# Kernel tuning notes

Measured on AMD Instinct MI355X. Metric: run time of the kernel, lower is better.

## Reference

```python
import jax, jax.numpy as jnp
import numpy as np

H = 8
D_MODEL = 512
D_K = D_MODEL // H
NEG = -1e9


def setup_inputs() -> dict:
    key = jax.random.key(0)
    ks = jax.random.split(key, 11)
    B, S = 2, 2048
    scale = 1.0 / np.sqrt(D_MODEL)
    inp = {
        'query': jax.random.normal(ks[0], (B, S, D_MODEL), dtype=jnp.float32),
        'key': jax.random.normal(ks[1], (B, S, D_MODEL), dtype=jnp.float32),
        'value': jax.random.normal(ks[2], (B, S, D_MODEL), dtype=jnp.float32),
        'Wq': jax.random.normal(ks[3], (D_MODEL, D_MODEL), dtype=jnp.float32) * scale,
        'bq': jnp.zeros((D_MODEL,), dtype=jnp.float32),
        'Wk': jax.random.normal(ks[4], (D_MODEL, D_MODEL), dtype=jnp.float32) * scale,
        'bk': jnp.zeros((D_MODEL,), dtype=jnp.float32),
        'Wv': jax.random.normal(ks[5], (D_MODEL, D_MODEL), dtype=jnp.float32) * scale,
        'bv': jnp.zeros((D_MODEL,), dtype=jnp.float32),
        'Wo': jax.random.normal(ks[6], (D_MODEL, D_MODEL), dtype=jnp.float32) * scale,
        'bo': jnp.zeros((D_MODEL,), dtype=jnp.float32),
    }
    return inp


def reference(query, key, value, Wq, bq, Wk, bk, Wv, bv, Wo, bo):
    B, S, _ = query.shape
    # QKV projections (nn.Linear: x @ W.T + b), split into heads -> [B, H, S, D_K]
    def proj(x, W, b):
        return (x @ W.T + b).reshape(B, S, H, D_K).transpose(0, 2, 1, 3)

    q = proj(query, Wq, bq)
    k = proj(key, Wk, bk)
    v = proj(value, Wv, bv)

    scores = jnp.einsum('bhqd,bhkd->bhqk', q, k) / jnp.sqrt(jnp.float32(D_K))
    # diagonal mask (mask=True): token cannot attend to itself
    diag = jnp.eye(S, dtype=bool)
    scores = jnp.where(diag, NEG, scores)

    p_attn = jax.nn.softmax(scores, axis=-1)  # [B, H, S, S]
    x = jnp.einsum('bhqk,bhkd->bhqd', p_attn, v)
    x = x.transpose(0, 2, 1, 3).reshape(B, S, H * D_K)
    return x @ Wo.T + bo
```

## Files before the change

### kernel.cpp

```cpp
#include <hip/hip_runtime.h>
#include <hip/hip_bf16.h>
#include <math.h>

#define NUM_H 8
#define DK    64
#define DM    512
#define SEQ   2048
#define NB    2
#define MROWS (NB*SEQ)

typedef unsigned short u16;
typedef unsigned int   u32;
typedef __attribute__((ext_vector_type(8))) __bf16 bf16x8;
typedef __attribute__((ext_vector_type(4))) float  f32x4;

__device__ __forceinline__ u16 f2bf(float v) {
    union { float f; u32 i; } x; x.f = v;
    u32 r = (x.i + 0x7FFFu + ((x.i >> 16) & 1u)) >> 16;
    return (u16)r;
}
__device__ __forceinline__ u16 f2h(float v) {
    union { _Float16 h; u16 u; } x; x.h = (_Float16)v; return x.u;
}
__device__ __forceinline__ float h2f(u16 u) {
    union { u16 u; _Float16 h; } x; x.u = u; return (float)x.h;
}
__device__ __forceinline__ bf16x8 ld_bf8(const u16* p) {
    union { uint4 u; bf16x8 v; } t;
    t.u = *(const uint4*)p;
    return t.v;
}
__device__ __forceinline__ uint4 pack8bf(const float* f) {
    uint4 o;
    o.x = (u32)f2bf(f[0]) | ((u32)f2bf(f[1]) << 16);
    o.y = (u32)f2bf(f[2]) | ((u32)f2bf(f[3]) << 16);
    o.z = (u32)f2bf(f[4]) | ((u32)f2bf(f[5]) << 16);
    o.w = (u32)f2bf(f[6]) | ((u32)f2bf(f[7]) << 16);
    return o;
}

__global__ __launch_bounds__(256) void convW(
    const float* __restrict__ Wq, const float* __restrict__ Wk,
    const float* __restrict__ Wv, const float* __restrict__ Wo,
    u16* __restrict__ Wscr)
{
    const int z = blockIdx.y;
    const float* src = (z == 0) ? Wq : (z == 1) ? Wk : (z == 2) ? Wv : Wo;
    u16* dst = Wscr + (size_t)z * 262144;
    int i = (blockIdx.x * 256 + threadIdx.x) * 8;
    float4 a = *(const float4*)(src + i);
    float4 b = *(const float4*)(src + i + 4);
    float f[8] = {a.x, a.y, a.z, a.w, b.x, b.y, b.z, b.w};
    *(uint4*)&dst[i] = pack8bf(f);
}

#define MODE_QK 0
#define MODE_VT 1
#define MODE_FIN 2

template<int MODE, bool INBF>
__device__ __forceinline__ void gemm_core(
    const void* __restrict__ Xv, const u16* __restrict__ Wb,
    const float* __restrict__ bias, void* __restrict__ outv,
    u16* As, u16* Bs, int row0, int col0)
{
    const int tid = threadIdx.x;
    const int lane = tid & 63, w = tid >> 6;
    const int ln15 = lane & 15, quad = lane >> 4;
    const int wm = (w >> 1) * 32, wn = (w & 1) * 32;

    f32x4 acc[2][2];
#pragma unroll
    for (int mt = 0; mt < 2; ++mt)
#pragma unroll
        for (int nt = 0; nt < 2; ++nt) acc[mt][nt] = (f32x4){0.f, 0.f, 0.f, 0.f};

    for (int kt = 0; kt < DM; kt += 64) {
        __syncthreads();
#pragma unroll
        for (int g = 0; g < 2; ++g) {
            int idx = g * 2048 + tid * 8;
            int r = idx >> 6, c = idx & 63;
            if (INBF) {
                *(uint4*)&As[r * 72 + c] =
                    *(const uint4*)((const u16*)Xv + (size_t)(row0 + r) * DM + kt + c);
            } else {
                const float* xp = (const float*)Xv + (size_t)(row0 + r) * DM + kt + c;
                float4 a = *(const float4*)xp;
                float4 b2 = *(const float4*)(xp + 4);
                float f[8] = {a.x, a.y, a.z, a.w, b2.x, b2.y, b2.z, b2.w};
                *(uint4*)&As[r * 72 + c] = pack8bf(f);
            }
        }
#pragma unroll
        for (int g = 0; g < 2; ++g) {
            int idx = g * 2048 + tid * 8;
            int r = idx >> 6, c = idx & 63;
            *(uint4*)&Bs[r * 72 + c] =
                *(const uint4*)(Wb + (size_t)(col0 + r) * DM + kt + c);
        }
        __syncthreads();

#pragma unroll
        for (int ks = 0; ks < 2; ++ks) {
            bf16x8 af[2], bfr[2];
#pragma unroll
            for (int mt = 0; mt < 2; ++mt)
                af[mt] = ld_bf8(&As[(wm + mt * 16 + ln15) * 72 + ks * 32 + quad * 8]);
#pragma unroll
            for (int nt = 0; nt < 2; ++nt)
                bfr[nt] = ld_bf8(&Bs[(wn + nt * 16 + ln15) * 72 + ks * 32 + quad * 8]);
#pragma unroll
            for (int mt = 0; mt < 2; ++mt)
#pragma unroll
                for (int nt = 0; nt < 2; ++nt)
                    acc[mt][nt] = __builtin_amdgcn_mfma_f32_16x16x32_bf16(
                        af[mt], bfr[nt], acc[mt][nt], 0, 0, 0);
        }
    }

    float bc[2];
#pragma unroll
    for (int nt = 0; nt < 2; ++nt) bc[nt] = bias[col0 + wn + nt * 16 + ln15];
    const int h = col0 >> 6;

    if (MODE == MODE_FIN) {
        float* outF = (float*)outv;
#pragma unroll
        for (int mt = 0; mt < 2; ++mt)
#pragma unroll
            for (int r = 0; r < 4; ++r) {
                int m = row0 + wm + mt * 16 + quad * 4 + r;
#pragma unroll
                for (int nt = 0; nt < 2; ++nt)
                    outF[(size_t)m * DM + col0 + wn + nt * 16 + ln15] = acc[mt][nt][r] + bc[nt];
            }
    } else if (MODE == MODE_QK) {
        u16* outB = (u16*)outv;
#pragma unroll
        for (int mt = 0; mt < 2; ++mt)
#pragma unroll
            for (int r = 0; r < 4; ++r) {
                int m = row0 + wm + mt * 16 + quad * 4 + r;
                int b = m >> 11, s2 = m & (SEQ - 1);
#pragma unroll
                for (int nt = 0; nt < 2; ++nt) {
                    int dk = wn + nt * 16 + ln15;
                    outB[((size_t)((b * NUM_H + h) * SEQ + s2)) * DK + dk] =
                        f2bf(acc[mt][nt][r] + bc[nt]);
                }
            }
    } else {
        u16* outB = (u16*)outv;
        __syncthreads();
#pragma unroll
        for (int mt = 0; mt < 2; ++mt)
#pragma unroll
            for (int nt = 0; nt < 2; ++nt) {
                int dk = wn + nt * 16 + ln15;
#pragma unroll
                for (int r = 0; r < 4; ++r) {
                    int sl = wm + mt * 16 + quad * 4 + r;
                    As[dk * 72 + sl] = f2bf(acc[mt][nt][r] + bc[nt]);
                }
            }
        __syncthreads();
        int dk = tid >> 2, ch = (tid & 3) * 16;
        int b = row0 >> 11, s0 = row0 & (SEQ - 1);
        size_t base = ((size_t)((b * NUM_H + h) * DK + dk)) * SEQ + s0 + ch;
        *(uint4*)&outB[base]     = *(const uint4*)&As[dk * 72 + ch];
        *(uint4*)&outB[base + 8] = *(const uint4*)&As[dk * 72 + ch + 8];
    }
}

__global__ __launch_bounds__(256) void qkv_mfma(
    const float* __restrict__ xq, const float* __restrict__ xk, const float* __restrict__ xv,
    const u16* __restrict__ Wscr,
    const float* __restrict__ b0, const float* __restrict__ b1, const float* __restrict__ b2,
    u16* __restrict__ oQ, u16* __restrict__ oK, u16* __restrict__ oVt)
{
    __shared__ u16 As[64 * 72];
    __shared__ u16 Bs[64 * 72];
    const int row0 = blockIdx.x * 64, col0 = blockIdx.y * 64;
    const int z = blockIdx.z;
    const u16* W = Wscr + (size_t)z * 262144;
    if (z == 2)
        gemm_core<MODE_VT, false>(xv, W, b2, oVt, As, Bs, row0, col0);
    else if (z == 0)
        gemm_core<MODE_QK, false>(xq, W, b0, oQ, As, Bs, row0, col0);
    else
        gemm_core<MODE_QK, false>(xk, W, b1, oK, As, Bs, row0, col0);
}

__global__ __launch_bounds__(256) void final_mfma(
    const u16* __restrict__ X, const u16* __restrict__ Wbf,
    const float* __restrict__ bias, float* __restrict__ out)
{
    __shared__ u16 As[64 * 72];
    __shared__ u16 Bs[64 * 72];
    gemm_core<MODE_FIN, true>(X, Wbf, bias, out, As, Bs,
                              blockIdx.x * 64, blockIdx.y * 64);
}

#define LSTR 72
__global__ __launch_bounds__(256) void attn_mfma(
    const u16* __restrict__ Qg, const u16* __restrict__ Kg,
    const u16* __restrict__ Vtg, u16* __restrict__ Pd, float* __restrict__ Cl)
{
    __shared__ u16 Klds[64 * LSTR];
    __shared__ u16 Vtlds[64 * LSTR];
    __shared__ u16 Pls[64 * LSTR];

    const int tid = threadIdx.x;
    const int lane = tid & 63;
    const int w = tid >> 6;
    const int ln15 = lane & 15;
    const int quad = lane >> 4;
    const int bh = blockIdx.y;
    const int b = bh >> 3, h = bh & 7;
    const int qb = blockIdx.x * 64;
    const int z = blockIdx.z;
    const int k0 = z * (SEQ / 2), k1 = k0 + SEQ / 2;

    const u16* Qp = Qg + (size_t)bh * SEQ * DK;
    const u16* Kp = Kg + (size_t)bh * SEQ * DK;
    const u16* Vp = Vtg + (size_t)bh * DK * SEQ;

    const int qrowA = qb + w * 16 + ln15;
    const bf16x8 qa0 = ld_bf8(&Qp[(size_t)qrowA * DK + quad * 8]);
    const bf16x8 qa1 = ld_bf8(&Qp[(size_t)qrowA * DK + 32 + quad * 8]);

    f32x4 O[4];
    float l_i[4] = {0.f, 0.f, 0.f, 0.f};
#pragma unroll
    for (int nt = 0; nt < 4; ++nt) O[nt] = (f32x4){0.f, 0.f, 0.f, 0.f};

    const int sr = tid >> 3;
    const int scl = (tid & 7) * 8;

    for (int kt = k0; kt < k1; kt += 64) {
        __syncthreads();
        *(uint4*)&Klds[sr * LSTR + scl]         = *(const uint4*)&Kp[(size_t)(kt + sr) * DK + scl];
        *(uint4*)&Klds[(sr + 32) * LSTR + scl]  = *(const uint4*)&Kp[(size_t)(kt + sr + 32) * DK + scl];
        *(uint4*)&Vtlds[sr * LSTR + scl]        = *(const uint4*)&Vp[(size_t)sr * SEQ + kt + scl];
        *(uint4*)&Vtlds[(sr + 32) * LSTR + scl] = *(const uint4*)&Vp[(size_t)(sr + 32) * SEQ + kt + scl];
        __syncthreads();

        const bool diagt = (kt == qb);
#pragma unroll
        for (int nt2 = 0; nt2 < 4; ++nt2) {
            bf16x8 kb0 = ld_bf8(&Klds[(nt2 * 16 + ln15) * LSTR + quad * 8]);
            bf16x8 kb1 = ld_bf8(&Klds[(nt2 * 16 + ln15) * LSTR + 32 + quad * 8]);
            f32x4 zacc = (f32x4){0.f, 0.f, 0.f, 0.f};
            zacc = __builtin_amdgcn_mfma_f32_16x16x32_bf16(qa0, kb0, zacc, 0, 0, 0);
            zacc = __builtin_amdgcn_mfma_f32_16x16x32_bf16(qa1, kb1, zacc, 0, 0, 0);
#pragma unroll
            for (int r = 0; r < 4; ++r) {
                float e = __expf(fmaf(zacc[r], 0.125f, -4.0f));
                if (diagt && (nt2 * 16 + ln15 == w * 16 + quad * 4 + r)) e = 0.f;
                l_i[r] += e;
                Pls[(w * 16 + quad * 4 + r) * LSTR + nt2 * 16 + ln15] = f2bf(e);
            }
        }

        bf16x8 pa0 = ld_bf8(&Pls[(w * 16 + ln15) * LSTR + quad * 8]);
        bf16x8 pa1 = ld_bf8(&Pls[(w * 16 + ln15) * LSTR + 32 + quad * 8]);
#pragma unroll
        for (int nt = 0; nt < 4; ++nt) {
            bf16x8 vb0 = ld_bf8(&Vtlds[(nt * 16 + ln15) * LSTR + quad * 8]);
            bf16x8 vb1 = ld_bf8(&Vtlds[(nt * 16 + ln15) * LSTR + 32 + quad * 8]);
            O[nt] = __builtin_amdgcn_mfma_f32_16x16x32_bf16(pa0, vb0, O[nt], 0, 0, 0);
            O[nt] = __builtin_amdgcn_mfma_f32_16x16x32_bf16(pa1, vb1, O[nt], 0, 0, 0);
        }
    }

#pragma unroll
    for (int r = 0; r < 4; ++r) {
        float s = l_i[r];
        s += __shfl_xor(s, 1);
        s += __shfl_xor(s, 2);
        s += __shfl_xor(s, 4);
        s += __shfl_xor(s, 8);
        l_i[r] = s;
    }
    if (ln15 == 0) {
#pragma unroll
        for (int r = 0; r < 4; ++r)
            Cl[(size_t)z * 32768 + bh * SEQ + qb + w * 16 + quad * 4 + r] = l_i[r];
    }
#pragma unroll
    for (int r = 0; r < 4; ++r) {
        int s = qb + w * 16 + quad * 4 + r;
        size_t base = (size_t)z * 2097152 + ((size_t)(b * SEQ + s)) * DM + h * DK;
#pragma unroll
        for (int nt = 0; nt < 4; ++nt)
            Pd[base + nt * 16 + ln15] = f2h(O[nt][r] * 0.015625f);
    }
}

__global__ __launch_bounds__(256) void combine(
    const u16* __restrict__ Pd, const float* __restrict__ Cl, u16* __restrict__ C)
{
    int idx = (blockIdx.x * 256 + threadIdx.x) * 8;
    int row = idx >> 9, col = idx & 511;
    int b = row >> 11, s = row & (SEQ - 1), h = col >> 6;
    int bh = b * NUM_H + h;
    float lsum = Cl[bh * SEQ + s] + Cl[32768 + bh * SEQ + s];
    float sc = 64.f / lsum;
    uint4 u0 = *(const uint4*)&Pd[idx];
    uint4 u1 = *(const uint4*)&Pd[2097152 + idx];
    u32 a0[4] = {u0.x, u0.y, u0.z, u0.w};
    u32 a1[4] = {u1.x, u1.y, u1.z, u1.w};
    float f[8];
#pragma unroll
    for (int j = 0; j < 4; ++j) {
        f[2 * j]     = (h2f((u16)(a0[j] & 0xffff)) + h2f((u16)(a1[j] & 0xffff))) * sc;
        f[2 * j + 1] = (h2f((u16)(a0[j] >> 16))    + h2f((u16)(a1[j] >> 16)))    * sc;
    }
    *(uint4*)&C[idx] = pack8bf(f);
}

extern "C" void kernel_launch(void* const* d_in, const int* in_sizes, int n_in,
                              void* d_out, int out_size, void* d_ws, size_t ws_size,
                              hipStream_t stream) {
    const float* q  = (const float*)d_in[0];
    const float* k  = (const float*)d_in[1];
    const float* v  = (const float*)d_in[2];
    const float* Wq = (const float*)d_in[3];
    const float* bq = (const float*)d_in[4];
    const float* Wk = (const float*)d_in[5];
    const float* bk = (const float*)d_in[6];
    const float* Wv = (const float*)d_in[7];
    const float* bv = (const float*)d_in[8];
    const float* Wo = (const float*)d_in[9];
    const float* bo = (const float*)d_in[10];
    float* out = (float*)d_out;

    const size_t TSZ = (size_t)MROWS * DM;
    u16* Qb  = (u16*)d_ws;
    u16* Kb  = Qb + TSZ;
    u16* Vtb = Qb + 2 * TSZ;
    u16* CbU = Qb + 3 * TSZ;
    float* Cl  = (float*)CbU;
    u16*  Wscr = CbU + 131072;

    u16* Pd = (u16*)d_out;

    dim3 blk(256);
    hipLaunchKernelGGL(convW, dim3(128, 4), blk, 0, stream, Wq, Wk, Wv, Wo, Wscr);
    dim3 gq(MROWS / 64, DM / 64, 3);
    hipLaunchKernelGGL(qkv_mfma, gq, blk, 0, stream,
                       q, k, v, Wscr, bq, bk, bv, Qb, Kb, Vtb);
    dim3 ga(SEQ / 64, NB * NUM_H, 2);
    hipLaunchKernelGGL(attn_mfma, ga, blk, 0, stream, Qb, Kb, Vtb, Pd, Cl);
    hipLaunchKernelGGL(combine, dim3(1024), blk, 0, stream, Pd, Cl, Qb);
    dim3 gf(MROWS / 64, DM / 64);
    hipLaunchKernelGGL(final_mfma, gf, blk, 0, stream, Qb, Wscr + 3 * 262144, bo, out);
}
```

Measured before the change: 161.1 us.

## Keep attention probabilities in registers by transposing QK^T MFMA operand order

```diff
diff --git a/kernel.cpp b/kernel.cpp
--- a/kernel.cpp
+++ b/kernel.cpp
@@ -12,12 +12,11 @@
 typedef unsigned short u16;
 typedef unsigned int   u32;
 typedef __attribute__((ext_vector_type(8))) __bf16 bf16x8;
+typedef __attribute__((ext_vector_type(4))) short  s16x4;
 typedef __attribute__((ext_vector_type(4))) float  f32x4;
 
 __device__ __forceinline__ u16 f2bf(float v) {
-    union { float f; u32 i; } x; x.f = v;
-    u32 r = (x.i + 0x7FFFu + ((x.i >> 16) & 1u)) >> 16;
-    return (u16)r;
+    union { __bf16 h; u16 u; } x; x.h = (__bf16)v; return x.u;
 }
 __device__ __forceinline__ u16 f2h(float v) {
     union { _Float16 h; u16 u; } x; x.h = (_Float16)v; return x.u;
@@ -37,6 +36,15 @@
     o.z = (u32)f2bf(f[4]) | ((u32)f2bf(f[5]) << 16);
     o.w = (u32)f2bf(f[6]) | ((u32)f2bf(f[7]) << 16);
     return o;
+}
+
+__device__ __forceinline__ f32x4 mfma16bf(s16x4 a, s16x4 b, f32x4 c) {
+#if defined(__has_builtin) && __has_builtin(__builtin_amdgcn_mfma_f32_16x16x16bf16_1k)
+    return __builtin_amdgcn_mfma_f32_16x16x16bf16_1k(a, b, c, 0, 0, 0);
+#else
+    asm("v_mfma_f32_16x16x16_bf16 %0, %1, %2, %0" : "+v"(c) : "v"(a), "v"(b));
+    return c;
+#endif
 }
 
 __global__ __launch_bounds__(256) void convW(
@@ -209,7 +217,6 @@
 {
     __shared__ u16 Klds[64 * LSTR];
     __shared__ u16 Vtlds[64 * LSTR];
-    __shared__ u16 Pls[64 * LSTR];
 
     const int tid = threadIdx.x;
     const int lane = tid & 63;
@@ -226,12 +233,13 @@
     const u16* Kp = Kg + (size_t)bh * SEQ * DK;
     const u16* Vp = Vtg + (size_t)bh * DK * SEQ;
 
-    const int qrowA = qb + w * 16 + ln15;
-    const bf16x8 qa0 = ld_bf8(&Qp[(size_t)qrowA * DK + quad * 8]);
-    const bf16x8 qa1 = ld_bf8(&Qp[(size_t)qrowA * DK + 32 + quad * 8]);
+    const int myq = w * 16 + ln15;
+    const int qrow = qb + myq;
+    const bf16x8 qa0 = ld_bf8(&Qp[(size_t)qrow * DK + quad * 8]);
+    const bf16x8 qa1 = ld_bf8(&Qp[(size_t)qrow * DK + 32 + quad * 8]);
 
     f32x4 O[4];
-    float l_i[4] = {0.f, 0.f, 0.f, 0.f};
+    float lsum = 0.f;
 #pragma unroll
     for (int nt = 0; nt < 4; ++nt) O[nt] = (f32x4){0.f, 0.f, 0.f, 0.f};
 
@@ -247,47 +255,41 @@
         __syncthreads();
 
         const bool diagt = (kt == qb);
+        s16x4 pa[4];
 #pragma unroll
         for (int nt2 = 0; nt2 < 4; ++nt2) {
             bf16x8 kb0 = ld_bf8(&Klds[(nt2 * 16 + ln15) * LSTR + quad * 8]);
             bf16x8 kb1 = ld_bf8(&Klds[(nt2 * 16 + ln15) * LSTR + 32 + quad * 8]);
             f32x4 zacc = (f32x4){0.f, 0.f, 0.f, 0.f};
-            zacc = __builtin_amdgcn_mfma_f32_16x16x32_bf16(qa0, kb0, zacc, 0, 0, 0);
-            zacc = __builtin_amdgcn_mfma_f32_16x16x32_bf16(qa1, kb1, zacc, 0, 0, 0);
+            zacc = __builtin_amdgcn_mfma_f32_16x16x32_bf16(kb0, qa0, zacc, 0, 0, 0);
+            zacc = __builtin_amdgcn_mfma_f32_16x16x32_bf16(kb1, qa1, zacc, 0, 0, 0);
+            union { u16 u[4]; s16x4 v; } pk;
 #pragma unroll
             for (int r = 0; r < 4; ++r) {
                 float e = __expf(fmaf(zacc[r], 0.125f, -4.0f));
-                if (diagt && (nt2 * 16 + ln15 == w * 16 + quad * 4 + r)) e = 0.f;
-                l_i[r] += e;
-                Pls[(w * 16 + quad * 4 + r) * LSTR + nt2 * 16 + ln15] = f2bf(e);
-            }
-        }
-
-        bf16x8 pa0 = ld_bf8(&Pls[(w * 16 + ln15) * LSTR + quad * 8]);
-        bf16x8 pa1 = ld_bf8(&Pls[(w * 16 + ln15) * LSTR + 32 + quad * 8]);
+                if (diagt && (nt2 * 16 + quad * 4 + r == myq)) e = 0.f;
+                lsum += e;
+                pk.u[r] = f2bf(e);
+            }
+            pa[nt2] = pk.v;
+        }
+
+        const u16* vb_base = &Vtlds[ln15 * LSTR + quad * 4];
 #pragma unroll
         for (int nt = 0; nt < 4; ++nt) {
-            bf16x8 vb0 = ld_bf8(&Vtlds[(nt * 16 + ln15) * LSTR + quad * 8]);
-            bf16x8 vb1 = ld_bf8(&Vtlds[(nt * 16 + ln15) * LSTR + 32 + quad * 8]);
-            O[nt] = __builtin_amdgcn_mfma_f32_16x16x32_bf16(pa0, vb0, O[nt], 0, 0, 0);
-            O[nt] = __builtin_amdgcn_mfma_f32_16x16x32_bf16(pa1, vb1, O[nt], 0, 0, 0);
-        }
-    }
-
-#pragma unroll
-    for (int r = 0; r < 4; ++r) {
-        float s = l_i[r];
-        s += __shfl_xor(s, 1);
-        s += __shfl_xor(s, 2);
-        s += __shfl_xor(s, 4);
-        s += __shfl_xor(s, 8);
-        l_i[r] = s;
-    }
-    if (ln15 == 0) {
-#pragma unroll
-        for (int r = 0; r < 4; ++r)
-            Cl[(size_t)z * 32768 + bh * SEQ + qb + w * 16 + quad * 4 + r] = l_i[r];
-    }
+#pragma unroll
+            for (int nt2 = 0; nt2 < 4; ++nt2) {
+                s16x4 vb = *(const s16x4*)&vb_base[nt * 16 * LSTR + nt2 * 16];
+                O[nt] = mfma16bf(pa[nt2], vb, O[nt]);
+            }
+        }
+    }
+
+    lsum += __shfl_xor(lsum, 16);
+    lsum += __shfl_xor(lsum, 32);
+    if (quad == 0)
+        Cl[(size_t)z * 32768 + bh * SEQ + qb + myq] = lsum;
+
 #pragma unroll
     for (int r = 0; r < 4; ++r) {
         int s = qb + w * 16 + quad * 4 + r;
```

New measurement: 160.7 us. Within noise of the previous version (-0.2%).
